# Kernel tuning notes

Measured on AMD Instinct MI355X. Metric: run time of the kernel, lower is better.

Reference implementation:

```python
import jax, jax.numpy as jnp
import numpy as np

B, T, E, H = 2, 2048, 1024, 16
D = E // H          # head_size = 64
DF = 4 * E          # FFN inner dim


def setup_inputs() -> dict:
    key = jax.random.key(0)
    ks = jax.random.split(key, 10)
    s = E ** -0.5
    return {
        "x":  jax.random.normal(ks[0], (B, T, E), jnp.float32),
        "Wq": jax.random.normal(ks[1], (H, E, D), jnp.float32) * s,
        "Wk": jax.random.normal(ks[2], (H, E, D), jnp.float32) * s,
        "Wv": jax.random.normal(ks[3], (H, E, D), jnp.float32) * s,
        "Wo": jax.random.normal(ks[4], (E, E), jnp.float32) * s,
        "bo": jnp.zeros((E,), jnp.float32),
        "W1": jax.random.normal(ks[5], (E, DF), jnp.float32) * s,
        "b1": jnp.zeros((DF,), jnp.float32),
        "W2": jax.random.normal(ks[6], (DF, E), jnp.float32) * (DF ** -0.5),
        "b2": jnp.zeros((E,), jnp.float32),
    }


def reference(x, Wq, Wk, Wv, Wo, bo, W1, b1, W2, b2):
    Bx, Tx, C = x.shape
    # NOTE: source scales by C**-0.5 where C = n_embed (not head_size) -- faithful.
    scale = C ** -0.5
    q = jnp.einsum('btc,hcd->bhtd', x, Wq)
    k = jnp.einsum('btc,hcd->bhtd', x, Wk)
    v = jnp.einsum('btc,hcd->bhtd', x, Wv)
    scores = jnp.einsum('bhtd,bhsd->bhts', q, k) * scale   # [B,H,T,T]
    causal = jnp.tril(jnp.ones((Tx, Tx), bool))
    scores = jnp.where(causal, scores, -jnp.inf)
    attn = jax.nn.softmax(scores, axis=-1)
    out = jnp.einsum('bhts,bhsd->bhtd', attn, v)
    out = out.transpose(0, 2, 1, 3).reshape(Bx, Tx, C)     # concat heads
    x = x + (out @ Wo + bo)                                # residual + projection
    h = jax.nn.relu(x @ W1 + b1)
    x = x + (h @ W2 + b2)                                  # residual + FFN
    return x
```

## Files before the change

kernel.cpp:

```cpp
#include <hip/hip_runtime.h>

#define B_ 2
#define T_ 2048
#define E_ 1024
#define H_ 16
#define D_ 64
#define DF_ 4096
#define M_ (B_*T_)
#define NQKV_ 3072

typedef unsigned short u16;
typedef __attribute__((ext_vector_type(8))) short short8;
typedef __attribute__((ext_vector_type(4))) float f32x4;
typedef __attribute__((ext_vector_type(16))) float f32x16;

__device__ __forceinline__ u16 f2bf(float f) {
  unsigned u = __builtin_bit_cast(unsigned, f);
  u += 0x7FFFu + ((u >> 16) & 1u);
  return (u16)(u >> 16);
}
__device__ __forceinline__ unsigned cvtpk(float a, float b) {
  unsigned r;
  asm("v_cvt_pk_bf16_f32 %0, %1, %2" : "=v"(r) : "v"(a), "v"(b));
  return r;
}
__device__ __forceinline__ float bf2f(u16 u) {
  return __builtin_bit_cast(float, (unsigned)u << 16);
}
__device__ __forceinline__ float vmax16(const f32x16& v) {
  float a0 = fmaxf(v[0], v[1]),   a1 = fmaxf(v[2], v[3]);
  float a2 = fmaxf(v[4], v[5]),   a3 = fmaxf(v[6], v[7]);
  float a4 = fmaxf(v[8], v[9]),   a5 = fmaxf(v[10], v[11]);
  float a6 = fmaxf(v[12], v[13]), a7 = fmaxf(v[14], v[15]);
  float b0 = fmaxf(a0, a1), b1 = fmaxf(a2, a3), b2 = fmaxf(a4, a5), b3 = fmaxf(a6, a7);
  return fmaxf(fmaxf(b0, b1), fmaxf(b2, b3));
}
__device__ __forceinline__ float vsum16(const f32x16& v) {
  float a0 = v[0] + v[1],   a1 = v[2] + v[3];
  float a2 = v[4] + v[5],   a3 = v[6] + v[7];
  float a4 = v[8] + v[9],   a5 = v[10] + v[11];
  float a6 = v[12] + v[13], a7 = v[14] + v[15];
  float b0 = a0 + a1, b1 = a2 + a3, b2 = a4 + a5, b3 = a6 + a7;
  return (b0 + b1) + (b2 + b3);
}

__device__ __forceinline__ void gload_lds16(const u16* g, u16* l) {
  __builtin_amdgcn_global_load_lds((const __attribute__((address_space(1))) void*)g,
                                   (__attribute__((address_space(3))) void*)l, 16, 0, 0);
}

__global__ __launch_bounds__(256) void cast_bf16_kernel(const float* __restrict__ in,
                                                        u16* __restrict__ out, int n4) {
  int i = blockIdx.x * 256 + threadIdx.x;
  if (i >= n4) return;
  float4 v = ((const float4*)in)[i];
  uint2 r;
  r.x = cvtpk(v.x, v.y);
  r.y = cvtpk(v.z, v.w);
  ((uint2*)out)[i] = r;
}

__global__ __launch_bounds__(256) void transpose_cast_kernel(const float* __restrict__ in,
                                                             u16* __restrict__ out,
                                                             int R, int C, int outld) {
  __shared__ float tile[32][33];
  int z = blockIdx.z;
  int c0 = blockIdx.x * 32, r0 = blockIdx.y * 32;
  int tx = threadIdx.x & 31, ty = threadIdx.x >> 5;
  const float* ip = in + (size_t)z * R * C;
#pragma unroll
  for (int i = 0; i < 32; i += 8)
    tile[ty + i][tx] = ip[(size_t)(r0 + ty + i) * C + (c0 + tx)];
  __syncthreads();
#pragma unroll
  for (int i = 0; i < 32; i += 8)
    out[(size_t)(z * C + c0 + ty + i) * outld + (r0 + tx)] = f2bf(tile[tx][ty + i]);
}

__global__ __launch_bounds__(256) void transpose_u16_kernel(const u16* __restrict__ in,
                                                            u16* __restrict__ out,
                                                            int R, int C, int ldin) {
  __shared__ __attribute__((aligned(16))) u16 tile[64][72];
  int c0 = blockIdx.x * 64, r0 = blockIdx.y * 64;
  int t = threadIdx.x;
  int tr = t >> 4, tc = (t & 15) * 4;
#pragma unroll
  for (int i = 0; i < 4; i++)
    *(uint2*)&tile[tr + i * 16][tc] = *(const uint2*)&in[(size_t)(r0 + tr + i * 16) * ldin + c0 + tc];
  __syncthreads();
  int rr = (t & 15) * 4, cc0 = t >> 4;
#pragma unroll
  for (int i = 0; i < 4; i++) {
    int cc = cc0 + i * 16;
    u16 a = tile[rr][cc], b = tile[rr + 1][cc], c = tile[rr + 2][cc], d = tile[rr + 3][cc];
    uint2 v;
    v.x = (unsigned)a | ((unsigned)b << 16);
    v.y = (unsigned)c | ((unsigned)d << 16);
    *(uint2*)&out[(size_t)(c0 + cc) * R + r0 + rr] = v;
  }
}

template<int TM, int TN, bool BIAS, bool RELU, bool RES, bool OF32, bool OBF>
__global__ __launch_bounds__(256, 2)
void gemm_bt(const u16* __restrict__ A,
             const u16* __restrict__ Bt,
             int M, int N, int K, int lda, int ldb,
             const float* __restrict__ bias,
             const float* __restrict__ res,
             float* __restrict__ outf,
             u16* __restrict__ outb) {
  constexpr int MF = TM / 32;
  constexpr int NF = TN / 32;
  constexpr int ACH = TM / 32;
  constexpr int BCH = TN / 32;
  __shared__ __attribute__((aligned(16))) u16 As[2][TM][64];
  __shared__ __attribute__((aligned(16))) u16 Bs[2][TN][64];
  int m0 = blockIdx.y * TM, n0 = blockIdx.x * TN;
  int z = blockIdx.z;
  A  += (size_t)z * K;
  Bt += (size_t)z * K;
  if (OF32 && outf) outf += (size_t)z * M * N;
  if (OBF && outb)  outb += (size_t)z * M * N;
  int tid = threadIdx.x;
  int lane = tid & 63, w = tid >> 6;
  int wr = w >> 1, wc = w & 1;
  int lg = lane >> 4, lq = lane & 15;
  int srow8 = lane >> 3;
  int scolsw = ((lane & 7) ^ srow8) * 8;

  const u16* aSrcP[ACH];
  const u16* bSrcP[BCH];
#pragma unroll
  for (int j = 0; j < ACH; j++)
    aSrcP[j] = &A[(size_t)(m0 + w * (ACH * 8) + j * 8 + srow8) * lda + scolsw];
#pragma unroll
  for (int j = 0; j < BCH; j++)
    bSrcP[j] = &Bt[(size_t)(n0 + w * (BCH * 8) + j * 8 + srow8) * ldb + scolsw];

  auto stage = [&](int buf, int k0) {
#pragma unroll
    for (int j = 0; j < ACH; j++)
      gload_lds16(aSrcP[j] + k0, &As[buf][w * (ACH * 8) + j * 8][0]);
#pragma unroll
    for (int j = 0; j < BCH; j++)
      gload_lds16(bSrcP[j] + k0, &Bs[buf][w * (BCH * 8) + j * 8][0]);
  };

  f32x4 acc[MF][NF] = {};
  int lqx = lq & 7;

  stage(0, 0);
  __syncthreads();
  int cur = 0;
  for (int k0 = 0; k0 < K; k0 += 64) {
    if (k0 + 64 < K) stage(cur ^ 1, k0 + 64);
#pragma unroll
    for (int kk = 0; kk < 2; kk++) {
      short8 af[MF], bf[NF];
      int csw = ((lg + kk * 4) ^ lqx) * 8;
#pragma unroll
      for (int m = 0; m < MF; m++) af[m] = *(const short8*)&As[cur][wr * (TM / 2) + m * 16 + lq][csw];
#pragma unroll
      for (int n = 0; n < NF; n++) bf[n] = *(const short8*)&Bs[cur][wc * (TN / 2) + n * 16 + lq][csw];
#pragma unroll
      for (int m = 0; m < MF; m++)
#pragma unroll
        for (int n = 0; n < NF; n++)
          acc[m][n] = __builtin_amdgcn_mfma_f32_16x16x32_bf16(af[m], bf[n], acc[m][n], 0, 0, 0);
    }
    __syncthreads();
    cur ^= 1;
  }

#pragma unroll
  for (int m = 0; m < MF; m++)
#pragma unroll
    for (int n = 0; n < NF; n++) {
      int row = m0 + wr * (TM / 2) + m * 16 + lg * 4;
      int col = n0 + wc * (TN / 2) + n * 16 + lq;
      float bv = BIAS ? bias[col] : 0.f;
      float vv[4];
#pragma unroll
      for (int r = 0; r < 4; r++) {
        float v = acc[m][n][r];
        if (BIAS) v += bv;
        if (RES)  v += res[(size_t)(row + r) * N + col];
        if (RELU) v = fmaxf(v, 0.f);
        if (OF32) outf[(size_t)(row + r) * N + col] = v;
        vv[r] = v;
      }
      if (OBF) {
        unsigned p01 = cvtpk(vv[0], vv[1]);
        unsigned p23 = cvtpk(vv[2], vv[3]);
        outb[(size_t)(row + 0) * N + col] = (u16)p01;
        outb[(size_t)(row + 1) * N + col] = (u16)(p01 >> 16);
        outb[(size_t)(row + 2) * N + col] = (u16)p23;
        outb[(size_t)(row + 3) * N + col] = (u16)(p23 >> 16);
      }
    }
}

__global__ __launch_bounds__(256) void reduce2_kernel(const float* __restrict__ x1,
                                                      const u16* __restrict__ p0,
                                                      const u16* __restrict__ p1,
                                                      const float* __restrict__ b2,
                                                      float* __restrict__ out) {
  int i = blockIdx.x * 256 + threadIdx.x;
  float4 xv = ((const float4*)x1)[i];
  ushort4 a = ((const ushort4*)p0)[i];
  ushort4 b = ((const ushort4*)p1)[i];
  const float4 bb = *(const float4*)&b2[(i * 4) & (E_ - 1)];
  float4 r;
  r.x = xv.x + bf2f(a.x) + bf2f(b.x) + bb.x;
  r.y = xv.y + bf2f(a.y) + bf2f(b.y) + bb.y;
  r.z = xv.z + bf2f(a.z) + bf2f(b.z) + bb.z;
  r.w = xv.w + bf2f(a.w) + bf2f(b.w) + bb.w;
  ((float4*)out)[i] = r;
}

__global__ __launch_bounds__(256) void attn_kernel(const u16* __restrict__ qkv,
                                                   const u16* __restrict__ Vt,
                                                   u16* __restrict__ attn) {
  __shared__ __attribute__((aligned(16))) u16 Ks[2][64 * 64];
  __shared__ __attribute__((aligned(16))) u16 Vs[2][64 * 64];
  int bid = blockIdx.x;
  int pp = bid >> 8, rrb = bid & 255;
  int h  = rrb >> 4;
  int jj = rrb & 15;
  int b  = pp;
  int qt = pp ? (15 - jj) : jj;
  int tid = threadIdx.x;
  int lane = tid & 63, w = tid >> 6;
  int l31 = lane & 31, hh = lane >> 5;
  int q0w = qt * 128 + w * 32;
  int q_abs = q0w + l31;

  short8 qf[4];
  const u16* Qrow = qkv + (size_t)(b * T_ + q_abs) * NQKV_ + h * 64;
#pragma unroll
  for (int ks = 0; ks < 4; ks++) qf[ks] = *(const short8*)&Qrow[ks * 16 + hh * 8];

  const u16* Kbase  = qkv + (size_t)(b * T_) * NQKV_ + 1024 + h * 64;
  const u16* Vtbase = Vt + (size_t)(h * 64) * M_ + b * T_;

  int r0s = tid >> 3, c0s = tid & 7;
  int r1s = r0s + 32;
  unsigned kd0 = (unsigned)((r0s * 128 + c0s * 16) ^ ((r0s & 7) << 4));
  unsigned kd1 = (unsigned)((r1s * 128 + c0s * 16) ^ ((r1s & 7) << 4));
  const u16* Kg0 = &Kbase[(size_t)r0s * NQKV_ + c0s * 8];
  const u16* Kg1 = &Kbase[(size_t)r1s * NQKV_ + c0s * 8];
  const u16* Vg0 = &Vtbase[(size_t)r0s * M_ + c0s * 8];
  const u16* Vg1 = &Vtbase[(size_t)r1s * M_ + c0s * 8];

  f32x16 o[2] = {};
  float m_run = -__builtin_inff(), l_run = 0.f;
  const float SCL = 0.03125f;
  const int s_stop = qt * 128 + 128;

  uint4 kr0 = *(const uint4*)Kg0;
  uint4 kr1 = *(const uint4*)Kg1;
  uint4 vr0 = *(const uint4*)Vg0;
  uint4 vr1 = *(const uint4*)Vg1;
  *(uint4*)((char*)&Ks[0][0] + kd0) = kr0;
  *(uint4*)((char*)&Ks[0][0] + kd1) = kr1;
  *(uint4*)((char*)&Vs[0][0] + kd0) = vr0;
  *(uint4*)((char*)&Vs[0][0] + kd1) = vr1;
  kr0 = *(const uint4*)&Kg0[(size_t)64 * NQKV_];
  kr1 = *(const uint4*)&Kg1[(size_t)64 * NQKV_];
  vr0 = *(const uint4*)&Vg0[64];
  vr1 = *(const uint4*)&Vg1[64];
  __syncthreads();
  int cur = 0;

  for (int s0 = 0; s0 < s_stop; s0 += 64) {
    if (s0 + 64 < s_stop) {
      char* kb = (char*)&Ks[cur ^ 1][0];
      char* vb = (char*)&Vs[cur ^ 1][0];
      *(uint4*)(kb + kd0) = kr0;
      *(uint4*)(kb + kd1) = kr1;
      *(uint4*)(vb + kd0) = vr0;
      *(uint4*)(vb + kd1) = vr1;
      if (s0 + 128 < s_stop) {
        kr0 = *(const uint4*)&Kg0[(size_t)(s0 + 128) * NQKV_];
        kr1 = *(const uint4*)&Kg1[(size_t)(s0 + 128) * NQKV_];
        vr0 = *(const uint4*)&Vg0[s0 + 128];
        vr1 = *(const uint4*)&Vg1[s0 + 128];
      }
    }

    if (s0 <= q0w + 31) {
      const char* KsC = (const char*)&Ks[cur][0];
      const char* VsC = (const char*)&Vs[cur][0];

      f32x16 st[2];
      __builtin_amdgcn_s_setprio(1);
#pragma unroll
      for (int c = 0; c < 2; c++) {
        f32x16 acc = {};
        int key = c * 32 + l31;
#pragma unroll
        for (int ks = 0; ks < 4; ks++) {
          unsigned off = (unsigned)((key * 128 + ks * 32 + hh * 16) ^ ((key & 7) << 4));
          short8 kf = *(const short8*)(KsC + off);
          acc = __builtin_amdgcn_mfma_f32_32x32x16_bf16(kf, qf[ks], acc, 0, 0, 0);
        }
        st[c] = acc;
      }
      __builtin_amdgcn_s_setprio(0);

      if (s0 + 63 > q0w) {
#pragma unroll
        for (int c = 0; c < 2; c++)
#pragma unroll
          for (int r = 0; r < 16; r++) {
            int key = s0 + c * 32 + (r & 3) + 8 * (r >> 2) + 4 * hh;
            st[c][r] = (key > q_abs) ? -__builtin_inff() : st[c][r];
          }
      }
      float tmax = fmaxf(vmax16(st[0]), vmax16(st[1]));
      tmax = fmaxf(tmax, __shfl_xor(tmax, 32));

      if (!__all(tmax - m_run <= 256.0f)) {
        float newm = fmaxf(m_run, tmax);
        float fac = __expf((m_run - newm) * SCL);
        l_run *= fac;
        o[0] *= fac;
        o[1] *= fac;
        m_run = newm;
      }
      float nm = -m_run * SCL;
#pragma unroll
      for (int c = 0; c < 2; c++)
#pragma unroll
        for (int r = 0; r < 16; r++)
          st[c][r] = __expf(fmaf(st[c][r], SCL, nm));
      float psum = vsum16(st[0]) + vsum16(st[1]);
      psum += __shfl_xor(psum, 32);
      l_run += psum;

      unsigned wds[2][8];
#pragma unroll
      for (int c = 0; c < 2; c++)
#pragma unroll
        for (int i = 0; i < 8; i++)
          wds[c][i] = cvtpk(st[c][2 * i], st[c][2 * i + 1]);

      __builtin_amdgcn_s_setprio(1);
#pragma unroll
      for (int ks16 = 0; ks16 < 4; ks16++) {
        int c = ks16 >> 1, e = ks16 & 1;
        unsigned send0 = hh ? wds[c][4 * e]     : wds[c][4 * e + 2];
        unsigned send1 = hh ? wds[c][4 * e + 1] : wds[c][4 * e + 3];
        unsigned recv0 = (unsigned)__shfl_xor((int)send0, 32);
        unsigned recv1 = (unsigned)__shfl_xor((int)send1, 32);
        uint4 fw;
        fw.x = hh ? recv0 : wds[c][4 * e];
        fw.y = hh ? recv1 : wds[c][4 * e + 1];
        fw.z = hh ? wds[c][4 * e + 2] : recv0;
        fw.w = hh ? wds[c][4 * e + 3] : recv1;
        short8 pf = __builtin_bit_cast(short8, fw);
#pragma unroll
        for (int dc = 0; dc < 2; dc++) {
          int d = dc * 32 + l31;
          unsigned off = (unsigned)((d * 128 + ks16 * 32 + hh * 16) ^ ((d & 7) << 4));
          short8 vf = *(const short8*)(VsC + off);
          o[dc] = __builtin_amdgcn_mfma_f32_32x32x16_bf16(vf, pf, o[dc], 0, 0, 0);
        }
      }
      __builtin_amdgcn_s_setprio(0);
    }

    __syncthreads();
    cur ^= 1;
  }

  float inv = 1.f / l_run;
  const size_t orow = (size_t)(b * T_ + q_abs) * E_ + h * 64;
#pragma unroll
  for (int dc = 0; dc < 2; dc++)
#pragma unroll
    for (int a = 0; a < 4; a++) {
      float e0 = o[dc][4 * a] * inv,     e1 = o[dc][4 * a + 1] * inv;
      float e2 = o[dc][4 * a + 2] * inv, e3 = o[dc][4 * a + 3] * inv;
      uint2 r;
      r.x = cvtpk(e0, e1);
      r.y = cvtpk(e2, e3);
      *(uint2*)&attn[orow + dc * 32 + 8 * a + 4 * hh] = r;
    }
}

extern "C" void kernel_launch(void* const* d_in, const int* in_sizes, int n_in,
                              void* d_out, int out_size, void* d_ws, size_t ws_size,
                              hipStream_t stream) {
  const float* x  = (const float*)d_in[0];
  const float* Wq = (const float*)d_in[1];
  const float* Wk = (const float*)d_in[2];
  const float* Wv = (const float*)d_in[3];
  const float* Wo = (const float*)d_in[4];
  const float* bo = (const float*)d_in[5];
  const float* W1 = (const float*)d_in[6];
  const float* b1 = (const float*)d_in[7];
  const float* W2 = (const float*)d_in[8];
  const float* b2 = (const float*)d_in[9];
  float* out = (float*)d_out;

  const size_t MB = 1048576;
  char* ws = (char*)d_ws;
  u16* xb    = (u16*)(ws + 0);
  u16* WqkvT = (u16*)(ws + 8 * MB);
  u16* WoT   = (u16*)(ws + 14 * MB);
  u16* W1T   = (u16*)(ws + 16 * MB);
  u16* W2T   = (u16*)(ws + 24 * MB);
  u16* qkv   = (u16*)(ws + 32 * MB);
  u16* attn  = (u16*)(ws + 56 * MB);
  float* x1  = (float*)(ws + 64 * MB);
  u16* Vtb   = (u16*)(ws + 64 * MB);
  u16* x1b   = (u16*)(ws + 0);
  u16* hbuf  = (u16*)(ws + 32 * MB);
  u16* pbuf  = (u16*)(ws + 0);

  cast_bf16_kernel<<<(M_ * E_ / 4 + 255) / 256, 256, 0, stream>>>(x, xb, M_ * E_ / 4);
  transpose_cast_kernel<<<dim3(2, 32, 16),  256, 0, stream>>>(Wq, WqkvT,                E_, D_, E_);
  transpose_cast_kernel<<<dim3(2, 32, 16),  256, 0, stream>>>(Wk, WqkvT + 1024 * 1024,  E_, D_, E_);
  transpose_cast_kernel<<<dim3(2, 32, 16),  256, 0, stream>>>(Wv, WqkvT + 2048 * 1024,  E_, D_, E_);
  transpose_cast_kernel<<<dim3(32, 32, 1),  256, 0, stream>>>(Wo, WoT, E_, E_, E_);
  transpose_cast_kernel<<<dim3(128, 32, 1), 256, 0, stream>>>(W1, W1T, E_, DF_, E_);
  transpose_cast_kernel<<<dim3(32, 128, 1), 256, 0, stream>>>(W2, W2T, DF_, E_, DF_);

  gemm_bt<128,128,false,false,false,false,true><<<dim3(NQKV_ / 128, M_ / 128), 256, 0, stream>>>(
      xb, WqkvT, M_, NQKV_, E_, E_, E_, nullptr, nullptr, nullptr, qkv);

  transpose_u16_kernel<<<dim3(E_ / 64, M_ / 64), 256, 0, stream>>>(qkv + 2048, Vtb, M_, E_, NQKV_);

  attn_kernel<<<B_ * H_ * (T_ / 128), 256, 0, stream>>>(qkv, Vtb, attn);

  gemm_bt<64,128,true,false,true,true,true><<<dim3(E_ / 128, M_ / 64), 256, 0, stream>>>(
      attn, WoT, M_, E_, E_, E_, E_, bo, x, x1, x1b);
  gemm_bt<128,128,true,true,false,false,true><<<dim3(DF_ / 128, M_ / 128), 256, 0, stream>>>(
      x1b, W1T, M_, DF_, E_, E_, E_, b1, nullptr, nullptr, hbuf);
  gemm_bt<128,128,false,false,false,false,true><<<dim3(E_ / 128, M_ / 128, 2), 256, 0, stream>>>(
      hbuf, W2T, M_, E_, DF_ / 2, DF_, DF_, nullptr, nullptr, nullptr, pbuf);
  reduce2_kernel<<<M_ * E_ / 4 / 256, 256, 0, stream>>>(x1, pbuf, pbuf + (size_t)M_ * E_, b2, out);
}
```

Before: 238.6 us.

## Split attention key tiles across two wave groups and merge softmax partials

The attention block grows from 4 to 8 waves. Waves are split into two parity groups that process alternate 64-key tiles for the same query rows. Each group keeps its own running max, sum and output, and at the end the partials are merged through shared memory by reusing the K/V buffers. Each thread now loads one row of the K/V tile instead of two. The exponentials switch to raw v_exp_f32 with a log2e-folded scale. This aims to increase wave-level parallelism and hide latency in the causal attention loop, at the cost of an extra merge step, more registers per block and a tighter occupancy bound.

```diff
diff --git a/kernel.cpp b/kernel.cpp
--- a/kernel.cpp
+++ b/kernel.cpp
@@ -22,6 +22,11 @@
 __device__ __forceinline__ unsigned cvtpk(float a, float b) {
   unsigned r;
   asm("v_cvt_pk_bf16_f32 %0, %1, %2" : "=v"(r) : "v"(a), "v"(b));
+  return r;
+}
+__device__ __forceinline__ float exp2a(float x) {
+  float r;
+  asm("v_exp_f32 %0, %1" : "=v"(r) : "v"(x));
   return r;
 }
 __device__ __forceinline__ float bf2f(u16 u) {
@@ -218,11 +223,12 @@
   ((float4*)out)[i] = r;
 }
 
-__global__ __launch_bounds__(256) void attn_kernel(const u16* __restrict__ qkv,
-                                                   const u16* __restrict__ Vt,
-                                                   u16* __restrict__ attn) {
+__global__ __launch_bounds__(512, 4) void attn_kernel(const u16* __restrict__ qkv,
+                                                      const u16* __restrict__ Vt,
+                                                      u16* __restrict__ attn) {
   __shared__ __attribute__((aligned(16))) u16 Ks[2][64 * 64];
   __shared__ __attribute__((aligned(16))) u16 Vs[2][64 * 64];
+  __shared__ float ml[4][2][32];
   int bid = blockIdx.x;
   int pp = bid >> 8, rrb = bid & 255;
   int h  = rrb >> 4;
@@ -231,8 +237,10 @@
   int qt = pp ? (15 - jj) : jj;
   int tid = threadIdx.x;
   int lane = tid & 63, w = tid >> 6;
+  int qg = w & 3;
+  int par = w >> 2;
   int l31 = lane & 31, hh = lane >> 5;
-  int q0w = qt * 128 + w * 32;
+  int q0w = qt * 128 + qg * 32;
   int q_abs = q0w + l31;
 
   short8 qf[4];
@@ -244,51 +252,35 @@
   const u16* Vtbase = Vt + (size_t)(h * 64) * M_ + b * T_;
 
   int r0s = tid >> 3, c0s = tid & 7;
-  int r1s = r0s + 32;
   unsigned kd0 = (unsigned)((r0s * 128 + c0s * 16) ^ ((r0s & 7) << 4));
-  unsigned kd1 = (unsigned)((r1s * 128 + c0s * 16) ^ ((r1s & 7) << 4));
   const u16* Kg0 = &Kbase[(size_t)r0s * NQKV_ + c0s * 8];
-  const u16* Kg1 = &Kbase[(size_t)r1s * NQKV_ + c0s * 8];
   const u16* Vg0 = &Vtbase[(size_t)r0s * M_ + c0s * 8];
-  const u16* Vg1 = &Vtbase[(size_t)r1s * M_ + c0s * 8];
 
   f32x16 o[2] = {};
   float m_run = -__builtin_inff(), l_run = 0.f;
-  const float SCL = 0.03125f;
+  const float SCL2 = 0.045084223f;
   const int s_stop = qt * 128 + 128;
 
   uint4 kr0 = *(const uint4*)Kg0;
-  uint4 kr1 = *(const uint4*)Kg1;
   uint4 vr0 = *(const uint4*)Vg0;
-  uint4 vr1 = *(const uint4*)Vg1;
   *(uint4*)((char*)&Ks[0][0] + kd0) = kr0;
-  *(uint4*)((char*)&Ks[0][0] + kd1) = kr1;
   *(uint4*)((char*)&Vs[0][0] + kd0) = vr0;
-  *(uint4*)((char*)&Vs[0][0] + kd1) = vr1;
   kr0 = *(const uint4*)&Kg0[(size_t)64 * NQKV_];
-  kr1 = *(const uint4*)&Kg1[(size_t)64 * NQKV_];
   vr0 = *(const uint4*)&Vg0[64];
-  vr1 = *(const uint4*)&Vg1[64];
   __syncthreads();
   int cur = 0;
 
   for (int s0 = 0; s0 < s_stop; s0 += 64) {
     if (s0 + 64 < s_stop) {
-      char* kb = (char*)&Ks[cur ^ 1][0];
-      char* vb = (char*)&Vs[cur ^ 1][0];
-      *(uint4*)(kb + kd0) = kr0;
-      *(uint4*)(kb + kd1) = kr1;
-      *(uint4*)(vb + kd0) = vr0;
-      *(uint4*)(vb + kd1) = vr1;
+      *(uint4*)((char*)&Ks[cur ^ 1][0] + kd0) = kr0;
+      *(uint4*)((char*)&Vs[cur ^ 1][0] + kd0) = vr0;
       if (s0 + 128 < s_stop) {
         kr0 = *(const uint4*)&Kg0[(size_t)(s0 + 128) * NQKV_];
-        kr1 = *(const uint4*)&Kg1[(size_t)(s0 + 128) * NQKV_];
         vr0 = *(const uint4*)&Vg0[s0 + 128];
-        vr1 = *(const uint4*)&Vg1[s0 + 128];
-      }
-    }
-
-    if (s0 <= q0w + 31) {
+      }
+    }
+
+    if (((s0 >> 6) & 1) == par && s0 <= q0w + 31) {
       const char* KsC = (const char*)&Ks[cur][0];
       const char* VsC = (const char*)&Vs[cur][0];
 
@@ -322,18 +314,18 @@
 
       if (!__all(tmax - m_run <= 256.0f)) {
         float newm = fmaxf(m_run, tmax);
-        float fac = __expf((m_run - newm) * SCL);
+        float fac = exp2a((m_run - newm) * SCL2);
         l_run *= fac;
         o[0] *= fac;
         o[1] *= fac;
         m_run = newm;
       }
-      float nm = -m_run * SCL;
+      float nm2 = -m_run * SCL2;
 #pragma unroll
       for (int c = 0; c < 2; c++)
 #pragma unroll
         for (int r = 0; r < 16; r++)
-          st[c][r] = __expf(fmaf(st[c][r], SCL, nm));
+          st[c][r] = exp2a(fmaf(st[c][r], SCL2, nm2));
       float psum = vsum16(st[0]) + vsum16(st[1]);
       psum += __shfl_xor(psum, 32);
       l_run += psum;
@@ -374,19 +366,50 @@
     cur ^= 1;
   }
 
-  float inv = 1.f / l_run;
-  const size_t orow = (size_t)(b * T_ + q_abs) * E_ + h * 64;
-#pragma unroll
-  for (int dc = 0; dc < 2; dc++)
-#pragma unroll
-    for (int a = 0; a < 4; a++) {
-      float e0 = o[dc][4 * a] * inv,     e1 = o[dc][4 * a + 1] * inv;
-      float e2 = o[dc][4 * a + 2] * inv, e3 = o[dc][4 * a + 3] * inv;
+  if (w >= 4) {
+    char* mb = (w < 6) ? ((char*)&Ks[0][0] + (w - 4) * 8192)
+                       : ((char*)&Vs[0][0] + (w - 6) * 8192);
+#pragma unroll
+    for (int g = 0; g < 8; g++) {
+      float4 v4;
+      v4.x = o[g >> 2][(g & 3) * 4];
+      v4.y = o[g >> 2][(g & 3) * 4 + 1];
+      v4.z = o[g >> 2][(g & 3) * 4 + 2];
+      v4.w = o[g >> 2][(g & 3) * 4 + 3];
+      *(float4*)(mb + g * 1024 + lane * 16) = v4;
+    }
+    if (hh == 0) {
+      ml[qg][0][l31] = m_run;
+      ml[qg][1][l31] = l_run;
+    }
+  }
+  __syncthreads();
+  if (w < 4) {
+    const char* mb = (qg < 2) ? ((const char*)&Ks[0][0] + qg * 8192)
+                              : ((const char*)&Vs[0][0] + (qg - 2) * 8192);
+    float m1 = ml[qg][0][l31];
+    float l1 = ml[qg][1][l31];
+    float mn = fmaxf(m_run, m1);
+    float f0 = exp2a((m_run - mn) * SCL2);
+    float f1 = exp2a((m1 - mn) * SCL2);
+    float ln = l_run * f0 + l1 * f1;
+    float inv = 1.f / ln;
+    float g0 = f0 * inv, g1 = f1 * inv;
+    const size_t orow = (size_t)(b * T_ + q_abs) * E_ + h * 64;
+#pragma unroll
+    for (int g = 0; g < 8; g++) {
+      float4 o1 = *(const float4*)(mb + g * 1024 + lane * 16);
+      int dc = g >> 2, a = g & 3;
+      float e0 = o[dc][4 * a]     * g0 + o1.x * g1;
+      float e1 = o[dc][4 * a + 1] * g0 + o1.y * g1;
+      float e2 = o[dc][4 * a + 2] * g0 + o1.z * g1;
+      float e3 = o[dc][4 * a + 3] * g0 + o1.w * g1;
       uint2 r;
       r.x = cvtpk(e0, e1);
       r.y = cvtpk(e2, e3);
       *(uint2*)&attn[orow + dc * 32 + 8 * a + 4 * hh] = r;
     }
+  }
 }
 
 extern "C" void kernel_launch(void* const* d_in, const int* in_sizes, int n_in,
@@ -432,7 +455,7 @@
 
   transpose_u16_kernel<<<dim3(E_ / 64, M_ / 64), 256, 0, stream>>>(qkv + 2048, Vtb, M_, E_, NQKV_);
 
-  attn_kernel<<<B_ * H_ * (T_ / 128), 256, 0, stream>>>(qkv, Vtb, attn);
+  attn_kernel<<<B_ * H_ * (T_ / 128), 512, 0, stream>>>(qkv, Vtb, attn);
 
   gemm_bt<64,128,true,false,true,true,true><<<dim3(E_ / 128, M_ / 64), 256, 0, stream>>>(
       attn, WoT, M_, E_, E_, E_, E_, bo, x, x1, x1b);
```

Result: faster. 230.2 us (-3.5%).
